# Performance work log

Measured on AMD Instinct MI355X. Metric: run time of the kernel, lower is better.

The kernel has to match this reference:

```python
import jax, jax.numpy as jnp
import numpy as np

N_EMBD = 512
N_HEAD = 8
HEAD = N_EMBD // N_HEAD
EPS = 1e-5

def layernorm(x, g, b):
    mu = jnp.mean(x, axis=-1, keepdims=True)
    var = jnp.mean(jnp.square(x - mu), axis=-1, keepdims=True)
    return (x - mu) * jax.lax.rsqrt(var + EPS) * g + b

def setup_inputs() -> dict:
    key = jax.random.key(0)
    ks = jax.random.split(key, 12)
    B, T, C, H, D = 32, 512, N_EMBD, N_HEAD, HEAD
    s = lambda fan: 1.0 / np.sqrt(fan)
    return {
        "x": jax.random.normal(ks[0], (B, T, C), jnp.float32),
        "wq": jax.random.normal(ks[1], (H, C, D), jnp.float32) * s(C),
        "wk": jax.random.normal(ks[2], (H, C, D), jnp.float32) * s(C),
        "wv": jax.random.normal(ks[3], (H, C, D), jnp.float32) * s(C),
        "w_proj": jax.random.normal(ks[4], (C, C), jnp.float32) * s(C),
        "b_proj": jnp.zeros((C,), jnp.float32),
        "w1": jax.random.normal(ks[5], (C, 4 * C), jnp.float32) * s(C),
        "b1": jnp.zeros((4 * C,), jnp.float32),
        "w2": jax.random.normal(ks[6], (4 * C, C), jnp.float32) * s(4 * C),
        "b2": jnp.zeros((C,), jnp.float32),
        "ln1_g": jnp.ones((C,), jnp.float32),
        "ln1_b": jnp.zeros((C,), jnp.float32),
        "ln2_g": jnp.ones((C,), jnp.float32),
        "ln2_b": jnp.zeros((C,), jnp.float32),
    }

def reference(x, wq, wk, wv, w_proj, b_proj, w1, b1, w2, b2, ln1_g, ln1_b, ln2_g, ln2_b):
    B, T, C = x.shape
    h = layernorm(x, ln1_g, ln1_b)
    q = jnp.einsum('btc,hcd->bhtd', h, wq)
    k = jnp.einsum('btc,hcd->bhtd', h, wk)
    v = jnp.einsum('btc,hcd->bhtd', h, wv)
    # NB: original scales by n_embd**-0.5 (C), not head_size
    scores = jnp.einsum('bhtd,bhsd->bhts', q, k) * (C ** -0.5)
    causal = jnp.tril(jnp.ones((T, T), bool))
    scores = jnp.where(causal, scores, -jnp.inf)
    attn = jax.nn.softmax(scores, axis=-1)
    o = jnp.einsum('bhts,bhsd->bhtd', attn, v)  # [B,H,T,D]
    o = jnp.transpose(o, (0, 2, 1, 3)).reshape(B, T, C)  # concat heads
    x = x + o @ w_proj + b_proj
    h2 = layernorm(x, ln2_g, ln2_b)
    ffn = jax.nn.relu(h2 @ w1 + b1) @ w2 + b2
    return x + ffn
```

## Files before the change

kernel.cpp:

```cpp
#include <hip/hip_runtime.h>
#include <hip/hip_bf16.h>


#define B_  32
#define T_  512
#define C_  512
#define H_  8
#define D_  64
#define BT  (B_*T_)
#define CF  2048

typedef __hip_bfloat16 bf16;
typedef __attribute__((ext_vector_type(8))) short bf16x8;
typedef __attribute__((ext_vector_type(4))) float f32x4;
typedef __attribute__((ext_vector_type(4))) short short4v;

__device__ __forceinline__ float bf2f(bf16 x) { return __bfloat162float(x); }
__device__ __forceinline__ bf16  f2bf(float x){ return __float2bfloat16(x); }
__device__ __forceinline__ short f2bf_bits(float f){
    bf16 h = __float2bfloat16(f);
    return *reinterpret_cast<short*>(&h);
}
__device__ __forceinline__ float bfbits2f(short s){
    unsigned u = ((unsigned)(unsigned short)s) << 16;
    return __uint_as_float(u);
}

#define AS_G __attribute__((address_space(1)))
#define AS_L __attribute__((address_space(3)))

__global__ __launch_bounds__(256) void transpose_all(const float* __restrict__ wq,
                                                     const float* __restrict__ wk,
                                                     const float* __restrict__ wv,
                                                     const float* __restrict__ wproj,
                                                     const float* __restrict__ w1,
                                                     const float* __restrict__ w2,
                                                     bf16* __restrict__ wt)
{
    const int t = blockIdx.x;
    const float* src; int K, Nn, k0, n0; size_t dstoff;
    if (t < 192) {
        const int which = t / 64, w = t % 64, hh = w >> 3, kt = w & 7;
        src = (which == 0 ? wq : which == 1 ? wk : wv) + (size_t)hh * 512 * 64;
        K = 512; Nn = 64; k0 = kt * 64; n0 = 0;
        dstoff = (size_t)(which * 512 + hh * 64) * 512;
    } else if (t < 256) {
        const int i = t - 192;
        src = wproj; K = 512; Nn = 512; n0 = (i & 7) * 64; k0 = (i >> 3) * 64;
        dstoff = (size_t)1536 * 512;
    } else if (t < 512) {
        const int i = t - 256;
        src = w1; K = 512; Nn = 2048; n0 = (i & 31) * 64; k0 = (i >> 5) * 64;
        dstoff = (size_t)2048 * 512;
    } else {
        const int i = t - 512;
        src = w2; K = 2048; Nn = 512; n0 = (i & 7) * 64; k0 = (i >> 3) * 64;
        dstoff = (size_t)2048 * 512 + (size_t)2048 * 512;
    }

    __shared__ float tl[64][65];
    const int tid = threadIdx.x;
    #pragma unroll
    for (int j = 0; j < 16; ++j) {
        const int e = j * 256 + tid, r = e >> 6, c = e & 63;
        tl[r][c] = src[(size_t)(k0 + r) * Nn + n0 + c];
    }
    __syncthreads();
    #pragma unroll
    for (int j = 0; j < 16; ++j) {
        const int e = j * 256 + tid, n = e >> 6, kk = e & 63;
        wt[dstoff + (size_t)(n0 + n) * K + k0 + kk] = f2bf(tl[kk][n]);
    }
}

__global__ __launch_bounds__(256) void ln_kernel(const float* __restrict__ x,
                                                 const float* __restrict__ g,
                                                 const float* __restrict__ b,
                                                 bf16* __restrict__ out)
{
    const int row = blockIdx.x;
    const int tid = threadIdx.x;
    const float* xr = x + (size_t)row * C_;
    float v0 = xr[tid], v1 = xr[tid + 256];

    __shared__ float red[4];

    float s = v0 + v1;
    #pragma unroll
    for (int off = 32; off > 0; off >>= 1) s += __shfl_down(s, off, 64);
    if ((tid & 63) == 0) red[tid >> 6] = s;
    __syncthreads();
    const float mean = (red[0] + red[1] + red[2] + red[3]) * (1.0f / C_);
    __syncthreads();

    float d0 = v0 - mean, d1 = v1 - mean;
    float vs = d0 * d0 + d1 * d1;
    #pragma unroll
    for (int off = 32; off > 0; off >>= 1) vs += __shfl_down(vs, off, 64);
    if ((tid & 63) == 0) red[tid >> 6] = vs;
    __syncthreads();
    const float var  = (red[0] + red[1] + red[2] + red[3]) * (1.0f / C_);
    const float rstd = rsqrtf(var + 1e-5f);

    bf16* orow = out + (size_t)row * C_;
    orow[tid]       = f2bf(d0 * rstd * g[tid]       + b[tid]);
    orow[tid + 256] = f2bf(d1 * rstd * g[tid + 256] + b[tid + 256]);
}

template<bool QKV, bool RELU, bool OUT_BF16>
__global__ __launch_bounds__(256, 3) void mfma_gemm(const bf16* __restrict__ A,
                                                    const bf16* __restrict__ Bt,
                                                    const float* __restrict__ bias,
                                                    const float* __restrict__ res,
                                                    void* __restrict__ outp,
                                                    int N, int K)
{
    __shared__ __align__(16) bf16 As[128 * 64];
    __shared__ __align__(16) bf16 Bs[128 * 64];

    const int tid  = threadIdx.x;
    const int wave = tid >> 6, lane = tid & 63;
    const int l16  = lane & 15, quad = lane >> 4;
    const int wm   = wave >> 1, wn = wave & 1;
    const int tm   = blockIdx.y * 128, tn = blockIdx.x * 128;
    const bool vblk = QKV && (tn >= 1024);

    f32x4 acc[4][4];
    #pragma unroll
    for (int i = 0; i < 4; ++i)
        #pragma unroll
        for (int j = 0; j < 4; ++j) acc[i][j] = (f32x4){0.f, 0.f, 0.f, 0.f};

    for (int k0 = 0; k0 < K; k0 += 64) {
        __syncthreads();
        #pragma unroll
        for (int j = 0; j < 4; ++j) {
            const int g = j * 256 + tid;
            const int row = g >> 3, phys = g & 7;
            const int c = phys ^ (row & 7);
            __builtin_amdgcn_global_load_lds((const AS_G void*)(A  + (size_t)(tm + row) * K + k0 + c * 8),
                                             (AS_L void*)&As[(size_t)g * 8], 16, 0, 0);
            __builtin_amdgcn_global_load_lds((const AS_G void*)(Bt + (size_t)(tn + row) * K + k0 + c * 8),
                                             (AS_L void*)&Bs[(size_t)g * 8], 16, 0, 0);
        }
        __syncthreads();

        #pragma unroll
        for (int half = 0; half < 2; ++half) {
            bf16x8 af[4], bfr[4];
            #pragma unroll
            for (int mf = 0; mf < 4; ++mf) {
                const int r = wm * 64 + mf * 16 + l16;
                const int p = (half * 4 + quad) ^ (r & 7);
                af[mf] = *(const bf16x8*)&As[r * 64 + p * 8];
            }
            #pragma unroll
            for (int nf = 0; nf < 4; ++nf) {
                const int r = wn * 64 + nf * 16 + l16;
                const int p = (half * 4 + quad) ^ (r & 7);
                bfr[nf] = *(const bf16x8*)&Bs[r * 64 + p * 8];
            }
            if (vblk) {
                #pragma unroll
                for (int mf = 0; mf < 4; ++mf)
                    #pragma unroll
                    for (int nf = 0; nf < 4; ++nf)
                        acc[mf][nf] = __builtin_amdgcn_mfma_f32_16x16x32_bf16(af[mf], bfr[nf], acc[mf][nf], 0, 0, 0);
            } else {
                #pragma unroll
                for (int mf = 0; mf < 4; ++mf)
                    #pragma unroll
                    for (int nf = 0; nf < 4; ++nf)
                        acc[mf][nf] = __builtin_amdgcn_mfma_f32_16x16x32_bf16(bfr[nf], af[mf], acc[mf][nf], 0, 0, 0);
            }
        }
    }

    if (QKV) {
        bf16* qkv = (bf16*)outp;
        if (!vblk) {
            const int which = tn >> 9;
            bf16* dst = qkv + (size_t)which * (8u << 20);
            #pragma unroll
            for (int mf = 0; mf < 4; ++mf) {
                const int m = tm + wm * 64 + mf * 16 + l16;
                const int bb = m >> 9, t = m & 511;
                #pragma unroll
                for (int nf = 0; nf < 4; ++nf) {
                    const int nb = tn + wn * 64 + nf * 16 + quad * 4;
                    const int hh = (nb >> 6) & 7, dd = nb & 63;
                    short4v pk;
                    #pragma unroll
                    for (int r = 0; r < 4; ++r) pk[r] = f2bf_bits(acc[mf][nf][r]);
                    *(short4v*)&dst[((size_t)(bb * 8 + hh) * 512 + t) * 64 + dd] = pk;
                }
            }
        } else {
            bf16* dst = qkv + (size_t)2 * (8u << 20);
            #pragma unroll
            for (int mf = 0; mf < 4; ++mf) {
                const int mb = tm + wm * 64 + mf * 16 + quad * 4;
                const int bb = mb >> 9, t = mb & 511;
                #pragma unroll
                for (int nf = 0; nf < 4; ++nf) {
                    const int n = tn + wn * 64 + nf * 16 + l16;
                    const int hh = (n >> 6) & 7, dd = n & 63;
                    short4v pk;
                    #pragma unroll
                    for (int r = 0; r < 4; ++r) pk[r] = f2bf_bits(acc[mf][nf][r]);
                    *(short4v*)&dst[((size_t)(bb * 8 + hh) * 64 + dd) * 512 + t] = pk;
                }
            }
        }
    } else {
        #pragma unroll
        for (int mf = 0; mf < 4; ++mf) {
            const int m = tm + wm * 64 + mf * 16 + l16;
            #pragma unroll
            for (int nf = 0; nf < 4; ++nf) {
                const int nb = tn + wn * 64 + nf * 16 + quad * 4;
                f32x4 a = acc[mf][nf];
                if (bias) a += *(const f32x4*)&bias[nb];
                if (RELU) {
                    #pragma unroll
                    for (int r = 0; r < 4; ++r) a[r] = fmaxf(a[r], 0.0f);
                }
                if (res)  a += *(const f32x4*)&res[(size_t)m * N + nb];
                if (OUT_BF16) {
                    short4v pk;
                    #pragma unroll
                    for (int r = 0; r < 4; ++r) pk[r] = f2bf_bits(a[r]);
                    *(short4v*)&((bf16*)outp)[(size_t)m * N + nb] = pk;
                } else {
                    *(f32x4*)&((float*)outp)[(size_t)m * N + nb] = a;
                }
            }
        }
    }
}

__global__ __launch_bounds__(256) void attn_kernel(const bf16* __restrict__ q,
                                                   const bf16* __restrict__ kM,
                                                   const bf16* __restrict__ vT,
                                                   bf16* __restrict__ o)
{
    __shared__ __align__(16) bf16 Ks[64][72];
    __shared__ __align__(16) bf16 Vt[64][72];
    __shared__ __align__(16) bf16 Pw[4][16][72];

    const int qt   = gridDim.x - 1 - blockIdx.x;
    const int bh   = blockIdx.y;
    const int tid  = threadIdx.x;
    const int wave = tid >> 6, lane = tid & 63;
    const int l16  = lane & 15, quad = lane >> 4;
    const int qw   = qt * 64 + wave * 16;

    const float scale = 0.04419417382415922f;
    bf16x8 qa[2];
    #pragma unroll
    for (int c = 0; c < 2; ++c) {
        const bf16* qp = q + ((size_t)bh * T_ + qw + l16) * 64 + c * 32 + quad * 8;
        bf16x8 t = *(const bf16x8*)qp;
        #pragma unroll
        for (int j = 0; j < 8; ++j) t[j] = f2bf_bits(bfbits2f(t[j]) * scale);
        qa[c] = t;
    }

    float m_i[4], l_i[4];
    f32x4 Of[4];
    #pragma unroll
    for (int r = 0; r < 4; ++r) { m_i[r] = -1e30f; l_i[r] = 0.0f; }
    #pragma unroll
    for (int f = 0; f < 4; ++f) Of[f] = (f32x4){0.f, 0.f, 0.f, 0.f};

    for (int kt = 0; kt <= qt; ++kt) {
        const int k0 = kt * 64;
        __syncthreads();
        #pragma unroll
        for (int c2 = 0; c2 < 2; ++c2) {
            const int ch = tid + c2 * 256;
            const int row = ch >> 3, e8 = (ch & 7) * 8;
            *(uint4*)&Ks[row][e8] = *(const uint4*)(kM + ((size_t)bh * T_ + k0 + row) * 64 + e8);
            *(uint4*)&Vt[row][e8] = *(const uint4*)(vT + ((size_t)bh * 64 + row) * T_ + k0 + e8);
        }
        __syncthreads();

        f32x4 Sf[4];
        #pragma unroll
        for (int kf = 0; kf < 4; ++kf) {
            bf16x8 b0 = *(const bf16x8*)&Ks[kf * 16 + l16][quad * 8];
            bf16x8 b1 = *(const bf16x8*)&Ks[kf * 16 + l16][32 + quad * 8];
            f32x4 z = (f32x4){0.f, 0.f, 0.f, 0.f};
            z = __builtin_amdgcn_mfma_f32_16x16x32_bf16(qa[0], b0, z, 0, 0, 0);
            z = __builtin_amdgcn_mfma_f32_16x16x32_bf16(qa[1], b1, z, 0, 0, 0);
            Sf[kf] = z;
        }

        if (kt == qt) {
            #pragma unroll
            for (int kf = 0; kf < 4; ++kf)
                #pragma unroll
                for (int r = 0; r < 4; ++r)
                    if (k0 + kf * 16 + l16 > qw + quad * 4 + r) Sf[kf][r] = -1e30f;
        }

        float mnew[4], alpha[4];
        #pragma unroll
        for (int r = 0; r < 4; ++r) {
            float v = fmaxf(fmaxf(Sf[0][r], Sf[1][r]), fmaxf(Sf[2][r], Sf[3][r]));
            v = fmaxf(v, __shfl_xor(v, 1, 64));
            v = fmaxf(v, __shfl_xor(v, 2, 64));
            v = fmaxf(v, __shfl_xor(v, 4, 64));
            v = fmaxf(v, __shfl_xor(v, 8, 64));
            mnew[r]  = fmaxf(m_i[r], v);
            alpha[r] = __expf(m_i[r] - mnew[r]);
            m_i[r]   = mnew[r];
        }

        float rs[4] = {0.f, 0.f, 0.f, 0.f};
        #pragma unroll
        for (int kf = 0; kf < 4; ++kf) {
            #pragma unroll
            for (int r = 0; r < 4; ++r) {
                float p = __expf(Sf[kf][r] - mnew[r]);
                rs[r] += p;
                Pw[wave][quad * 4 + r][kf * 16 + l16] = f2bf(p);
            }
        }
        #pragma unroll
        for (int r = 0; r < 4; ++r) {
            rs[r] += __shfl_xor(rs[r], 1, 64);
            rs[r] += __shfl_xor(rs[r], 2, 64);
            rs[r] += __shfl_xor(rs[r], 4, 64);
            rs[r] += __shfl_xor(rs[r], 8, 64);
            l_i[r] = l_i[r] * alpha[r] + rs[r];
        }
        #pragma unroll
        for (int f = 0; f < 4; ++f)
            #pragma unroll
            for (int r = 0; r < 4; ++r)
                Of[f][r] *= alpha[r];

        bf16x8 pa0 = *(const bf16x8*)&Pw[wave][l16][quad * 8];
        bf16x8 pa1 = *(const bf16x8*)&Pw[wave][l16][32 + quad * 8];
        #pragma unroll
        for (int f = 0; f < 4; ++f) {
            bf16x8 vb0 = *(const bf16x8*)&Vt[f * 16 + l16][quad * 8];
            bf16x8 vb1 = *(const bf16x8*)&Vt[f * 16 + l16][32 + quad * 8];
            Of[f] = __builtin_amdgcn_mfma_f32_16x16x32_bf16(pa0, vb0, Of[f], 0, 0, 0);
            Of[f] = __builtin_amdgcn_mfma_f32_16x16x32_bf16(pa1, vb1, Of[f], 0, 0, 0);
        }
    }

    const int b = bh >> 3, hh = bh & 7;
    #pragma unroll
    for (int r = 0; r < 4; ++r) {
        const float inv = 1.0f / l_i[r];
        const int t = qw + quad * 4 + r;
        #pragma unroll
        for (int f = 0; f < 4; ++f)
            o[((size_t)b * T_ + t) * C_ + hh * 64 + f * 16 + l16] = f2bf(Of[f][r] * inv);
    }
}

extern "C" void kernel_launch(void* const* d_in, const int* in_sizes, int n_in,
                              void* d_out, int out_size, void* d_ws, size_t ws_size,
                              hipStream_t stream)
{
    const float* x     = (const float*)d_in[0];
    const float* wq    = (const float*)d_in[1];
    const float* wk    = (const float*)d_in[2];
    const float* wv    = (const float*)d_in[3];
    const float* wproj = (const float*)d_in[4];
    const float* bproj = (const float*)d_in[5];
    const float* w1    = (const float*)d_in[6];
    const float* b1    = (const float*)d_in[7];
    const float* w2    = (const float*)d_in[8];
    const float* b2    = (const float*)d_in[9];
    const float* ln1g  = (const float*)d_in[10];
    const float* ln1b  = (const float*)d_in[11];
    const float* ln2g  = (const float*)d_in[12];
    const float* ln2b  = (const float*)d_in[13];

    char* ws = (char*)d_ws;
    bf16*  h    = (bf16*)(ws + 0);
    bf16*  q    = (bf16*)(ws + ((size_t)16 << 20));
    bf16*  k    = (bf16*)(ws + ((size_t)32 << 20));
    bf16*  v    = (bf16*)(ws + ((size_t)48 << 20));
    bf16*  mid  = (bf16*)(ws + 0);
    bf16*  o    = (bf16*)(ws + ((size_t)64 << 20));
    bf16*  h2   = (bf16*)(ws + ((size_t)80 << 20));
    bf16*  wt   = (bf16*)(ws + ((size_t)96 << 20));
    bf16*  projt = wt + (size_t)1536 * 512;
    bf16*  w1t   = wt + (size_t)2048 * 512;
    bf16*  w2t   = wt + (size_t)4096 * 512;
    float* x1    = (float*)d_out;

    transpose_all<<<768, 256, 0, stream>>>(wq, wk, wv, wproj, w1, w2, wt);

    ln_kernel<<<BT, 256, 0, stream>>>(x, ln1g, ln1b, h);

    mfma_gemm<true,  false, true ><<<dim3(12, 128), 256, 0, stream>>>(h, wt, nullptr, nullptr, q, 1536, 512);

    attn_kernel<<<dim3(8, B_ * H_), 256, 0, stream>>>(q, k, v, o);

    mfma_gemm<false, false, false><<<dim3(4, 128), 256, 0, stream>>>(o, projt, bproj, x, x1, 512, 512);

    ln_kernel<<<BT, 256, 0, stream>>>(x1, ln2g, ln2b, h2);

    mfma_gemm<false, true,  true ><<<dim3(16, 128), 256, 0, stream>>>(h2, w1t, b1, nullptr, mid, 2048, 512);

    mfma_gemm<false, false, false><<<dim3(4, 128), 256, 0, stream>>>(mid, w2t, b2, x1, (float*)d_out, 512, 2048);
}
```

Measured before the change: 392.5 us.

## Load GEMM fragments directly from global memory into registers, dropping LDS staging

The MFMA GEMM no longer stages A and B tiles through shared memory with global_load_lds and barriers. Each wave now loads its bf16x8 fragments straight from global memory into registers, double-buffered across the two 32-wide k halves so the next loads overlap the current MFMAs. This removes the LDS traffic and the __syncthreads, but gives up cross-wave reuse: every wave reloads rows it shares with the other waves, so the kernel relies on L1/L2 hits. The launch-bounds occupancy hint is also removed, which may raise register use.

```diff
diff --git a/kernel.cpp b/kernel.cpp
--- a/kernel.cpp
+++ b/kernel.cpp
@@ -25,9 +25,6 @@
     unsigned u = ((unsigned)(unsigned short)s) << 16;
     return __uint_as_float(u);
 }
-
-#define AS_G __attribute__((address_space(1)))
-#define AS_L __attribute__((address_space(3)))
 
 __global__ __launch_bounds__(256) void transpose_all(const float* __restrict__ wq,
                                                      const float* __restrict__ wk,
@@ -108,16 +105,13 @@
 }
 
 template<bool QKV, bool RELU, bool OUT_BF16>
-__global__ __launch_bounds__(256, 3) void mfma_gemm(const bf16* __restrict__ A,
-                                                    const bf16* __restrict__ Bt,
-                                                    const float* __restrict__ bias,
-                                                    const float* __restrict__ res,
-                                                    void* __restrict__ outp,
-                                                    int N, int K)
+__global__ __launch_bounds__(256) void mfma_gemm(const bf16* __restrict__ A,
+                                                 const bf16* __restrict__ Bt,
+                                                 const float* __restrict__ bias,
+                                                 const float* __restrict__ res,
+                                                 void* __restrict__ outp,
+                                                 int N, int K)
 {
-    __shared__ __align__(16) bf16 As[128 * 64];
-    __shared__ __align__(16) bf16 Bs[128 * 64];
-
     const int tid  = threadIdx.x;
     const int wave = tid >> 6, lane = tid & 63;
     const int l16  = lane & 15, quad = lane >> 4;
@@ -125,55 +119,53 @@
     const int tm   = blockIdx.y * 128, tn = blockIdx.x * 128;
     const bool vblk = QKV && (tn >= 1024);
 
+    const bf16* aB = A  + (size_t)(tm + wm * 64 + l16) * K + quad * 8;
+    const bf16* bB = Bt + (size_t)(tn + wn * 64 + l16) * K + quad * 8;
+
     f32x4 acc[4][4];
     #pragma unroll
     for (int i = 0; i < 4; ++i)
         #pragma unroll
         for (int j = 0; j < 4; ++j) acc[i][j] = (f32x4){0.f, 0.f, 0.f, 0.f};
 
+    auto do_mfma = [&](bf16x8 (&af)[4], bf16x8 (&bfr)[4]) {
+        if (vblk) {
+            #pragma unroll
+            for (int mf = 0; mf < 4; ++mf)
+                #pragma unroll
+                for (int nf = 0; nf < 4; ++nf)
+                    acc[mf][nf] = __builtin_amdgcn_mfma_f32_16x16x32_bf16(af[mf], bfr[nf], acc[mf][nf], 0, 0, 0);
+        } else {
+            #pragma unroll
+            for (int mf = 0; mf < 4; ++mf)
+                #pragma unroll
+                for (int nf = 0; nf < 4; ++nf)
+                    acc[mf][nf] = __builtin_amdgcn_mfma_f32_16x16x32_bf16(bfr[nf], af[mf], acc[mf][nf], 0, 0, 0);
+        }
+    };
+
+    bf16x8 a0[4], b0[4], a1[4], b1[4];
+    #pragma unroll
+    for (int f = 0; f < 4; ++f) {
+        a0[f] = *(const bf16x8*)(aB + (size_t)f * 16 * K);
+        b0[f] = *(const bf16x8*)(bB + (size_t)f * 16 * K);
+    }
+
     for (int k0 = 0; k0 < K; k0 += 64) {
-        __syncthreads();
-        #pragma unroll
-        for (int j = 0; j < 4; ++j) {
-            const int g = j * 256 + tid;
-            const int row = g >> 3, phys = g & 7;
-            const int c = phys ^ (row & 7);
-            __builtin_amdgcn_global_load_lds((const AS_G void*)(A  + (size_t)(tm + row) * K + k0 + c * 8),
-                                             (AS_L void*)&As[(size_t)g * 8], 16, 0, 0);
-            __builtin_amdgcn_global_load_lds((const AS_G void*)(Bt + (size_t)(tn + row) * K + k0 + c * 8),
-                                             (AS_L void*)&Bs[(size_t)g * 8], 16, 0, 0);
-        }
-        __syncthreads();
-
-        #pragma unroll
-        for (int half = 0; half < 2; ++half) {
-            bf16x8 af[4], bfr[4];
-            #pragma unroll
-            for (int mf = 0; mf < 4; ++mf) {
-                const int r = wm * 64 + mf * 16 + l16;
-                const int p = (half * 4 + quad) ^ (r & 7);
-                af[mf] = *(const bf16x8*)&As[r * 64 + p * 8];
+        #pragma unroll
+        for (int f = 0; f < 4; ++f) {
+            a1[f] = *(const bf16x8*)(aB + (size_t)f * 16 * K + k0 + 32);
+            b1[f] = *(const bf16x8*)(bB + (size_t)f * 16 * K + k0 + 32);
+        }
+        do_mfma(a0, b0);
+        if (k0 + 64 < K) {
+            #pragma unroll
+            for (int f = 0; f < 4; ++f) {
+                a0[f] = *(const bf16x8*)(aB + (size_t)f * 16 * K + k0 + 64);
+                b0[f] = *(const bf16x8*)(bB + (size_t)f * 16 * K + k0 + 64);
             }
-            #pragma unroll
-            for (int nf = 0; nf < 4; ++nf) {
-                const int r = wn * 64 + nf * 16 + l16;
-                const int p = (half * 4 + quad) ^ (r & 7);
-                bfr[nf] = *(const bf16x8*)&Bs[r * 64 + p * 8];
-            }
-            if (vblk) {
-                #pragma unroll
-                for (int mf = 0; mf < 4; ++mf)
-                    #pragma unroll
-                    for (int nf = 0; nf < 4; ++nf)
-                        acc[mf][nf] = __builtin_amdgcn_mfma_f32_16x16x32_bf16(af[mf], bfr[nf], acc[mf][nf], 0, 0, 0);
-            } else {
-                #pragma unroll
-                for (int mf = 0; mf < 4; ++mf)
-                    #pragma unroll
-                    for (int nf = 0; nf < 4; ++nf)
-                        acc[mf][nf] = __builtin_amdgcn_mfma_f32_16x16x32_bf16(bfr[nf], af[mf], acc[mf][nf], 0, 0, 0);
-            }
-        }
+        }
+        do_mfma(a1, b1);
     }
 
     if (QKV) {
```

New measurement: 600.1 us. +52.9%, slower.

## Double-buffer GEMM LDS tiles with register prefetch and BK=32

Applied to the files above, without the earlier changes.

Replaces the single-buffered 64-wide K tile loaded with global_load_lds by a double-buffered 32-wide K tile. The next tile is prefetched into registers during the MFMA work and then written to the alternate LDS buffer, which removes one barrier per iteration and overlaps global loads with compute. The swizzle is rebuilt for the 32-column layout. In exchange it uses more VGPRs for the prefetch registers, runs twice as many iterations with less work each, and gives up the direct-to-LDS loads.

```diff
diff --git a/kernel.cpp b/kernel.cpp
--- a/kernel.cpp
+++ b/kernel.cpp
@@ -25,9 +25,6 @@
     unsigned u = ((unsigned)(unsigned short)s) << 16;
     return __uint_as_float(u);
 }
-
-#define AS_G __attribute__((address_space(1)))
-#define AS_L __attribute__((address_space(3)))
 
 __global__ __launch_bounds__(256) void transpose_all(const float* __restrict__ wq,
                                                      const float* __restrict__ wk,
@@ -115,8 +112,8 @@
                                                     void* __restrict__ outp,
                                                     int N, int K)
 {
-    __shared__ __align__(16) bf16 As[128 * 64];
-    __shared__ __align__(16) bf16 Bs[128 * 64];
+    __shared__ __align__(16) bf16 As[2 * 128 * 32];
+    __shared__ __align__(16) bf16 Bs[2 * 128 * 32];
 
     const int tid  = threadIdx.x;
     const int wave = tid >> 6, lane = tid & 63;
@@ -125,54 +122,70 @@
     const int tm   = blockIdx.y * 128, tn = blockIdx.x * 128;
     const bool vblk = QKV && (tn >= 1024);
 
+    const int rowS = tid >> 2, pS = tid & 3;
+    const int c0 = pS ^ ((rowS >> 1) & 3);
+    const int c1 = pS ^ (((rowS + 64) >> 1) & 3);
+    const bf16* gA0 = A  + (size_t)(tm + rowS) * K + c0 * 8;
+    const bf16* gA1 = A  + (size_t)(tm + rowS + 64) * K + c1 * 8;
+    const bf16* gB0 = Bt + (size_t)(tn + rowS) * K + c0 * 8;
+    const bf16* gB1 = Bt + (size_t)(tn + rowS + 64) * K + c1 * 8;
+    const int ldsOff0 = rowS * 32 + pS * 8;
+    const int ldsOff1 = (rowS + 64) * 32 + pS * 8;
+
     f32x4 acc[4][4];
     #pragma unroll
     for (int i = 0; i < 4; ++i)
         #pragma unroll
         for (int j = 0; j < 4; ++j) acc[i][j] = (f32x4){0.f, 0.f, 0.f, 0.f};
 
-    for (int k0 = 0; k0 < K; k0 += 64) {
-        __syncthreads();
-        #pragma unroll
-        for (int j = 0; j < 4; ++j) {
-            const int g = j * 256 + tid;
-            const int row = g >> 3, phys = g & 7;
-            const int c = phys ^ (row & 7);
-            __builtin_amdgcn_global_load_lds((const AS_G void*)(A  + (size_t)(tm + row) * K + k0 + c * 8),
-                                             (AS_L void*)&As[(size_t)g * 8], 16, 0, 0);
-            __builtin_amdgcn_global_load_lds((const AS_G void*)(Bt + (size_t)(tn + row) * K + k0 + c * 8),
-                                             (AS_L void*)&Bs[(size_t)g * 8], 16, 0, 0);
-        }
-        __syncthreads();
-
-        #pragma unroll
-        for (int half = 0; half < 2; ++half) {
-            bf16x8 af[4], bfr[4];
-            #pragma unroll
-            for (int mf = 0; mf < 4; ++mf) {
-                const int r = wm * 64 + mf * 16 + l16;
-                const int p = (half * 4 + quad) ^ (r & 7);
-                af[mf] = *(const bf16x8*)&As[r * 64 + p * 8];
-            }
-            #pragma unroll
-            for (int nf = 0; nf < 4; ++nf) {
-                const int r = wn * 64 + nf * 16 + l16;
-                const int p = (half * 4 + quad) ^ (r & 7);
-                bfr[nf] = *(const bf16x8*)&Bs[r * 64 + p * 8];
-            }
-            if (vblk) {
+    uint4 pa0 = *(const uint4*)gA0, pa1 = *(const uint4*)gA1;
+    uint4 pb0 = *(const uint4*)gB0, pb1 = *(const uint4*)gB1;
+    *(uint4*)&As[ldsOff0] = pa0;  *(uint4*)&As[ldsOff1] = pa1;
+    *(uint4*)&Bs[ldsOff0] = pb0;  *(uint4*)&Bs[ldsOff1] = pb1;
+    __syncthreads();
+
+    const int nIter = K >> 5;
+    for (int it = 0; it < nIter; ++it) {
+        const int cur = (it & 1) * 4096, nxt = 4096 - cur;
+        const bool more = (it + 1 < nIter);
+
+        if (more) {
+            const int ko = (it + 1) << 5;
+            pa0 = *(const uint4*)(gA0 + ko);  pa1 = *(const uint4*)(gA1 + ko);
+            pb0 = *(const uint4*)(gB0 + ko);  pb1 = *(const uint4*)(gB1 + ko);
+        }
+
+        bf16x8 af[4], bfr[4];
+        #pragma unroll
+        for (int mf = 0; mf < 4; ++mf) {
+            const int r = wm * 64 + mf * 16 + l16;
+            const int p = quad ^ ((r >> 1) & 3);
+            af[mf] = *(const bf16x8*)&As[cur + r * 32 + p * 8];
+        }
+        #pragma unroll
+        for (int nf = 0; nf < 4; ++nf) {
+            const int r = wn * 64 + nf * 16 + l16;
+            const int p = quad ^ ((r >> 1) & 3);
+            bfr[nf] = *(const bf16x8*)&Bs[cur + r * 32 + p * 8];
+        }
+        if (vblk) {
+            #pragma unroll
+            for (int mf = 0; mf < 4; ++mf)
                 #pragma unroll
-                for (int mf = 0; mf < 4; ++mf)
-                    #pragma unroll
-                    for (int nf = 0; nf < 4; ++nf)
-                        acc[mf][nf] = __builtin_amdgcn_mfma_f32_16x16x32_bf16(af[mf], bfr[nf], acc[mf][nf], 0, 0, 0);
-            } else {
+                for (int nf = 0; nf < 4; ++nf)
+                    acc[mf][nf] = __builtin_amdgcn_mfma_f32_16x16x32_bf16(af[mf], bfr[nf], acc[mf][nf], 0, 0, 0);
+        } else {
+            #pragma unroll
+            for (int mf = 0; mf < 4; ++mf)
                 #pragma unroll
-                for (int mf = 0; mf < 4; ++mf)
-                    #pragma unroll
-                    for (int nf = 0; nf < 4; ++nf)
-                        acc[mf][nf] = __builtin_amdgcn_mfma_f32_16x16x32_bf16(bfr[nf], af[mf], acc[mf][nf], 0, 0, 0);
-            }
+                for (int nf = 0; nf < 4; ++nf)
+                    acc[mf][nf] = __builtin_amdgcn_mfma_f32_16x16x32_bf16(bfr[nf], af[mf], acc[mf][nf], 0, 0, 0);
+        }
+
+        if (more) {
+            *(uint4*)&As[nxt + ldsOff0] = pa0;  *(uint4*)&As[nxt + ldsOff1] = pa1;
+            *(uint4*)&Bs[nxt + ldsOff0] = pb0;  *(uint4*)&Bs[nxt + ldsOff1] = pb1;
+            __syncthreads();
         }
     }
 
```

After: 467.4 us. +19.1%, slower.

## Double-buffer GEMM LDS tiles with K-step 32 to overlap loads and MFMA

Applied to the files above, without the earlier changes.

Replaces the single 128x64 LDS tile per operand with two ping-pong 128x32 buffers, so global-to-LDS loads for the next K slice are issued before computing on the current one. Address pointers are precomputed once and the swizzle pattern is adapted to the 32-wide rows. This aims to hide global memory latency behind MFMA work, at the cost of more barriers per K element and smaller per-stage work. Total LDS use stays the same.

```diff
diff --git a/kernel.cpp b/kernel.cpp
--- a/kernel.cpp
+++ b/kernel.cpp
@@ -107,6 +107,51 @@
     orow[tid + 256] = f2bf(d1 * rstd * g[tid + 256] + b[tid + 256]);
 }
 
+
+#define STAGE(as, bs, k0)                                                                  \
+    do {                                                                                   \
+        __builtin_amdgcn_global_load_lds((const AS_G void*)(gA0 + (k0)),                   \
+                                         (AS_L void*)&as[d0], 16, 0, 0);                   \
+        __builtin_amdgcn_global_load_lds((const AS_G void*)(gA1 + (k0)),                   \
+                                         (AS_L void*)&as[d1], 16, 0, 0);                   \
+        __builtin_amdgcn_global_load_lds((const AS_G void*)(gB0 + (k0)),                   \
+                                         (AS_L void*)&bs[d0], 16, 0, 0);                   \
+        __builtin_amdgcn_global_load_lds((const AS_G void*)(gB1 + (k0)),                   \
+                                         (AS_L void*)&bs[d1], 16, 0, 0);                   \
+    } while (0)
+
+#define COMPUTE(as, bs)                                                                    \
+    do {                                                                                   \
+        bf16x8 af[4], bfr[4];                                                              \
+        _Pragma("unroll")                                                                  \
+        for (int mf = 0; mf < 4; ++mf) {                                                   \
+            const int r = wm * 64 + mf * 16 + l16;                                         \
+            const int p = quad ^ ((r >> 1) & 3);                                           \
+            af[mf] = *(const bf16x8*)&as[r * 32 + p * 8];                                  \
+        }                                                                                  \
+        _Pragma("unroll")                                                                  \
+        for (int nf = 0; nf < 4; ++nf) {                                                   \
+            const int r = wn * 64 + nf * 16 + l16;                                         \
+            const int p = quad ^ ((r >> 1) & 3);                                           \
+            bfr[nf] = *(const bf16x8*)&bs[r * 32 + p * 8];                                 \
+        }                                                                                  \
+        if (vblk) {                                                                        \
+            _Pragma("unroll")                                                              \
+            for (int mf = 0; mf < 4; ++mf)                                                 \
+                _Pragma("unroll")                                                          \
+                for (int nf = 0; nf < 4; ++nf)                                             \
+                    acc[mf][nf] = __builtin_amdgcn_mfma_f32_16x16x32_bf16(                 \
+                        af[mf], bfr[nf], acc[mf][nf], 0, 0, 0);                            \
+        } else {                                                                           \
+            _Pragma("unroll")                                                              \
+            for (int mf = 0; mf < 4; ++mf)                                                 \
+                _Pragma("unroll")                                                          \
+                for (int nf = 0; nf < 4; ++nf)                                             \
+                    acc[mf][nf] = __builtin_amdgcn_mfma_f32_16x16x32_bf16(                 \
+                        bfr[nf], af[mf], acc[mf][nf], 0, 0, 0);                            \
+        }                                                                                  \
+    } while (0)
+
 template<bool QKV, bool RELU, bool OUT_BF16>
 __global__ __launch_bounds__(256, 3) void mfma_gemm(const bf16* __restrict__ A,
                                                     const bf16* __restrict__ Bt,
@@ -115,8 +160,10 @@
                                                     void* __restrict__ outp,
                                                     int N, int K)
 {
-    __shared__ __align__(16) bf16 As[128 * 64];
-    __shared__ __align__(16) bf16 Bs[128 * 64];
+    __shared__ __align__(16) bf16 As0[128 * 32];
+    __shared__ __align__(16) bf16 Bs0[128 * 32];
+    __shared__ __align__(16) bf16 As1[128 * 32];
+    __shared__ __align__(16) bf16 Bs1[128 * 32];
 
     const int tid  = threadIdx.x;
     const int wave = tid >> 6, lane = tid & 63;
@@ -125,55 +172,33 @@
     const int tm   = blockIdx.y * 128, tn = blockIdx.x * 128;
     const bool vblk = QKV && (tn >= 1024);
 
+    const int rowS = tid >> 2, pS = tid & 3;
+    const int cA0 = pS ^ ((rowS >> 1) & 3);
+    const int cA1 = pS ^ (((rowS + 64) >> 1) & 3);
+    const bf16* gA0 = A  + (size_t)(tm + rowS) * K + cA0 * 8;
+    const bf16* gA1 = A  + (size_t)(tm + rowS + 64) * K + cA1 * 8;
+    const bf16* gB0 = Bt + (size_t)(tn + rowS) * K + cA0 * 8;
+    const bf16* gB1 = Bt + (size_t)(tn + rowS + 64) * K + cA1 * 8;
+    const int d0 = tid * 8;
+    const int d1 = (256 + tid) * 8;
+
     f32x4 acc[4][4];
     #pragma unroll
     for (int i = 0; i < 4; ++i)
         #pragma unroll
         for (int j = 0; j < 4; ++j) acc[i][j] = (f32x4){0.f, 0.f, 0.f, 0.f};
 
-    for (int k0 = 0; k0 < K; k0 += 64) {
+    STAGE(As0, Bs0, 0);
+    __syncthreads();
+
+    const int nIter = K >> 5;
+    for (int it = 0; it < nIter; it += 2) {
+        STAGE(As1, Bs1, (it + 1) << 5);
+        COMPUTE(As0, Bs0);
         __syncthreads();
-        #pragma unroll
-        for (int j = 0; j < 4; ++j) {
-            const int g = j * 256 + tid;
-            const int row = g >> 3, phys = g & 7;
-            const int c = phys ^ (row & 7);
-            __builtin_amdgcn_global_load_lds((const AS_G void*)(A  + (size_t)(tm + row) * K + k0 + c * 8),
-                                             (AS_L void*)&As[(size_t)g * 8], 16, 0, 0);
-            __builtin_amdgcn_global_load_lds((const AS_G void*)(Bt + (size_t)(tn + row) * K + k0 + c * 8),
-                                             (AS_L void*)&Bs[(size_t)g * 8], 16, 0, 0);
-        }
+        if (it + 2 < nIter) STAGE(As0, Bs0, (it + 2) << 5);
+        COMPUTE(As1, Bs1);
         __syncthreads();
-
-        #pragma unroll
-        for (int half = 0; half < 2; ++half) {
-            bf16x8 af[4], bfr[4];
-            #pragma unroll
-            for (int mf = 0; mf < 4; ++mf) {
-                const int r = wm * 64 + mf * 16 + l16;
-                const int p = (half * 4 + quad) ^ (r & 7);
-                af[mf] = *(const bf16x8*)&As[r * 64 + p * 8];
-            }
-            #pragma unroll
-            for (int nf = 0; nf < 4; ++nf) {
-                const int r = wn * 64 + nf * 16 + l16;
-                const int p = (half * 4 + quad) ^ (r & 7);
-                bfr[nf] = *(const bf16x8*)&Bs[r * 64 + p * 8];
-            }
-            if (vblk) {
-                #pragma unroll
-                for (int mf = 0; mf < 4; ++mf)
-                    #pragma unroll
-                    for (int nf = 0; nf < 4; ++nf)
-                        acc[mf][nf] = __builtin_amdgcn_mfma_f32_16x16x32_bf16(af[mf], bfr[nf], acc[mf][nf], 0, 0, 0);
-            } else {
-                #pragma unroll
-                for (int mf = 0; mf < 4; ++mf)
-                    #pragma unroll
-                    for (int nf = 0; nf < 4; ++nf)
-                        acc[mf][nf] = __builtin_amdgcn_mfma_f32_16x16x32_bf16(bfr[nf], af[mf], acc[mf][nf], 0, 0, 0);
-            }
-        }
     }
 
     if (QKV) {
```

Result: slower. 435.2 us (+10.9%).
